# Performance work log

Hardware: AMD Instinct MI355X
Metric: run time of the kernel (lower is better)

Reference implementation:

```python
import jax, jax.numpy as jnp
import numpy as np
import math

B, T, D, H = 2, 2048, 2048, 16
HD = D // H  # head_dim = 128


def setup_inputs() -> dict:
    key = jax.random.key(0)
    ks = jax.random.split(key, 9)
    s = 1.0 / math.sqrt(D)
    return {
        "x": jax.random.normal(ks[0], (B, T, D), dtype=jnp.float32),
        "Wq": jax.random.normal(ks[1], (D, D), dtype=jnp.float32) * s,
        "bq": jax.random.normal(ks[2], (D,), dtype=jnp.float32) * 0.01,
        "Wk": jax.random.normal(ks[3], (D, D), dtype=jnp.float32) * s,
        "bk": jax.random.normal(ks[4], (D,), dtype=jnp.float32) * 0.01,
        "Wv": jax.random.normal(ks[5], (D, D), dtype=jnp.float32) * s,
        "bv": jax.random.normal(ks[6], (D,), dtype=jnp.float32) * 0.01,
        "Wo": jax.random.normal(ks[7], (D, D), dtype=jnp.float32) * s,
        "bo": jax.random.normal(ks[8], (D,), dtype=jnp.float32) * 0.01,
    }


def reference(x, Wq, bq, Wk, bk, Wv, bv, Wo, bo):
    b, t, c = x.shape
    # projections; split heads: (B,T,D) -> (B,H,T,HD)
    def split_heads(y):
        return y.reshape(b, t, H, HD).transpose(0, 2, 1, 3)

    q = split_heads(x @ Wq + bq)
    k = split_heads(x @ Wk + bk)
    v = split_heads(x @ Wv + bv)

    scale = 1.0 / math.sqrt(HD)
    attn = jnp.einsum('bhqd,bhkd->bhqk', q, k) * scale  # (B,H,T,T)
    # causal mask (prefill path: past_k is None)
    causal = jnp.tril(jnp.ones((t, t), dtype=bool))
    attn = jnp.where(causal, attn, -jnp.inf)
    attn = jax.nn.softmax(attn, axis=-1)
    out = jnp.einsum('bhqk,bhkd->bhqd', attn, v)  # (B,H,T,HD)
    out = out.transpose(0, 2, 1, 3).reshape(b, t, c)
    out = out @ Wo + bo
    return (out, k, v)
```

## Files before the change

kernel.cpp:

```cpp
#include <hip/hip_runtime.h>
#include <hip/hip_bf16.h>

#define B_ 2
#define T_ 2048
#define D_ 2048
#define H_ 16
#define HD_ 128
#define M_ 4096

typedef __attribute__((ext_vector_type(8))) short short8;
typedef __attribute__((ext_vector_type(8))) __bf16 bf16x8;
typedef __attribute__((ext_vector_type(4))) float f32x4;
typedef __attribute__((ext_vector_type(4))) unsigned uint32x4;

__device__ __forceinline__ short f2bf(float f) {
  unsigned u = __builtin_bit_cast(unsigned, f);
  u += 0x7fffu + ((u >> 16) & 1u);
  return (short)(u >> 16);
}

__device__ __forceinline__ unsigned cvtpk(float lo, float hi) {
  unsigned r;
  asm("v_cvt_pk_bf16_f32 %0, %1, %2" : "=v"(r) : "v"(lo), "v"(hi));
  return r;
}

__device__ __forceinline__ float ex2(float x) {
  float r;
  asm("v_exp_f32 %0, %1" : "=v"(r) : "v"(x));
  return r;
}

__device__ __forceinline__ void gl_lds16(const void* g, void* l) {
  __builtin_amdgcn_global_load_lds(
      (const __attribute__((address_space(1))) unsigned int*)g,
      (__attribute__((address_space(3))) unsigned int*)l, 16, 0, 0);
}

__device__ __forceinline__ f32x4 mfma_bf16(short8 a, short8 b, f32x4 c) {
  return __builtin_amdgcn_mfma_f32_16x16x32_bf16(
      __builtin_bit_cast(bf16x8, a), __builtin_bit_cast(bf16x8, b), c, 0, 0, 0);
}

__device__ __forceinline__ float2 sw16f(float x) {
  float a = x, bv;
  asm("v_mov_b32 %0, %1" : "=v"(bv) : "v"(x));
  asm("v_permlane16_swap_b32 %0, %1" : "+v"(a), "+v"(bv));
  return make_float2(a, bv);
}
__device__ __forceinline__ float2 sw32f(float x) {
  float a = x, bv;
  asm("v_mov_b32 %0, %1" : "=v"(bv) : "v"(x));
  asm("v_permlane32_swap_b32 %0, %1" : "+v"(a), "+v"(bv));
  return make_float2(a, bv);
}
__device__ __forceinline__ void sw16u(unsigned x, unsigned& e, unsigned& o) {
  unsigned a = x, bv;
  asm("v_mov_b32 %0, %1" : "=v"(bv) : "v"(x));
  asm("v_permlane16_swap_b32 %0, %1" : "+v"(a), "+v"(bv));
  e = a; o = bv;
}
__device__ __forceinline__ void pl32u(unsigned& a, unsigned& b) {
  asm("v_permlane32_swap_b32 %0, %1" : "+v"(a), "+v"(b));
}

__global__ void prep_fused(const float* __restrict__ Wq, const float* __restrict__ Wk,
                           const float* __restrict__ Wv, const float* __restrict__ Wo,
                           const float* __restrict__ x,
                           short* __restrict__ wqkv, short* __restrict__ wo,
                           short* __restrict__ xb) {
  int z = blockIdx.z;
  int tx = threadIdx.x, ty = threadIdx.y;
  if (z == 4) {
    int n4 = M_ * D_ / 4;
    int i = (blockIdx.y * 64 + blockIdx.x) * 256 + ty * 32 + tx;
    int stride = 64 * 64 * 256;
    for (; i < n4; i += stride) {
      float4 v = ((const float4*)x)[i];
      short4 s;
      s.x = f2bf(v.x); s.y = f2bf(v.y); s.z = f2bf(v.z); s.w = f2bf(v.w);
      ((short4*)xb)[i] = s;
    }
    return;
  }
  __shared__ float t[32][33];
  const float* W = z == 0 ? Wq : z == 1 ? Wk : z == 2 ? Wv : Wo;
  short* dst = z < 3 ? wqkv + (size_t)z * D_ * D_ : wo;
  int n0 = blockIdx.x * 32, k0 = blockIdx.y * 32;
#pragma unroll
  for (int j = 0; j < 4; ++j)
    t[ty + j * 8][tx] = W[(size_t)(k0 + ty + j * 8) * D_ + n0 + tx];
  __syncthreads();
#pragma unroll
  for (int j = 0; j < 4; ++j)
    dst[(size_t)(n0 + ty + j * 8) * D_ + k0 + tx] = f2bf(t[tx][ty + j * 8]);
}

__global__ __launch_bounds__(512, 2) void gemm_qkv(
    const short* __restrict__ A, const short* __restrict__ Bt,
    const float* __restrict__ b0, const float* __restrict__ b1,
    const float* __restrict__ b2,
    short* __restrict__ q_o, short* __restrict__ k_o,
    float* __restrict__ kf_o, float* __restrict__ vf_o,
    short* __restrict__ vt_o) {
  __shared__ __attribute__((aligned(16))) char lds[2][57344];
  const int K = D_, NT = K / 64;

  int d = blockIdx.x;
  int lg = (d & 7) * 64 + (d >> 3);
  int m0 = (lg & 15) * 256, n0 = (lg >> 4) * 192;

  int tid = threadIdx.x, lane = tid & 63, wid = tid >> 6;
  int wm = wid >> 2, wn = wid & 3;
  int lr = lane & 15, g = lane >> 4;

  int rowA = tid >> 2;
  int cA = ((((tid & 3) << 4) ^ (((rowA >> 1) & 3) << 4)) >> 1);
  const short* aS = A + (size_t)(m0 + rowA) * K + cA;
  int rowB = tid >> 3;
  int cB = ((((tid & 7) << 4) ^ ((rowB & 7) << 4)) >> 1);
  const short* bS = Bt + (size_t)(n0 + rowB) * K + cB;
  char* ldsb = (char*)lds;

  auto stageA = [&](int ts, int kh) {
    char* dst = ldsb + (ts & 1) * 57344 + kh * 16384 + tid * 16;
    const short* s = aS + ts * 64 + kh * 32;
    gl_lds16(s, dst);
    gl_lds16(s + (size_t)128 * K, dst + 8192);
  };
  auto stageB = [&](int ts) {
    char* dst = ldsb + (ts & 1) * 57344 + 32768 + tid * 16;
    const short* s = bS + ts * 64;
    gl_lds16(s, dst);
    gl_lds16(s + (size_t)64 * K, dst + 8192);
    gl_lds16(s + (size_t)128 * K, dst + 16384);
  };

  int swzA = (g * 16) ^ (((lr >> 1) & 3) << 4);
  int aoff = (wm * 128 + lr) * 64 + swzA;
  int boff0 = (wn * 48 + lr) * 128 + ((g * 16) ^ ((lr & 7) << 4));
  int boff1 = (wn * 48 + lr) * 128 + ((64 + g * 16) ^ ((lr & 7) << 4));

  f32x4 acc[8][3] = {};

  stageA(0, 0); stageB(0); stageA(0, 1); stageA(1, 0);
  asm volatile("s_waitcnt vmcnt(4)" ::: "memory");
  __builtin_amdgcn_s_barrier();
  __builtin_amdgcn_sched_barrier(0);

#pragma unroll 1
  for (int t = 0; t < NT; ++t) {
    const char* base = ldsb + (t & 1) * 57344;
    int t1 = (t + 1 < NT) ? t + 1 : NT - 1;
    int t2 = (t + 2 < NT) ? t + 2 : NT - 1;
    short8 afr[8], bfr[3];

#pragma unroll
    for (int mi = 0; mi < 8; ++mi) afr[mi] = *(const short8*)(base + aoff + mi * 1024);
#pragma unroll
    for (int ni = 0; ni < 3; ++ni) bfr[ni] = *(const short8*)(base + 32768 + boff0 + ni * 2048);
    stageA(t1, 1); stageB(t1);
    __builtin_amdgcn_s_setprio(1);
#pragma unroll
    for (int mi = 0; mi < 8; ++mi)
#pragma unroll
      for (int ni = 0; ni < 3; ++ni)
        acc[mi][ni] = mfma_bf16(afr[mi], bfr[ni], acc[mi][ni]);
    __builtin_amdgcn_s_setprio(0);
    asm volatile("s_waitcnt vmcnt(7)" ::: "memory");
    __builtin_amdgcn_s_barrier();
    __builtin_amdgcn_sched_barrier(0);

#pragma unroll
    for (int mi = 0; mi < 8; ++mi) afr[mi] = *(const short8*)(base + 16384 + aoff + mi * 1024);
#pragma unroll
    for (int ni = 0; ni < 3; ++ni) bfr[ni] = *(const short8*)(base + 32768 + boff1 + ni * 2048);
    stageA(t2, 0);
    __builtin_amdgcn_s_setprio(1);
#pragma unroll
    for (int mi = 0; mi < 8; ++mi)
#pragma unroll
      for (int ni = 0; ni < 3; ++ni)
        acc[mi][ni] = mfma_bf16(afr[mi], bfr[ni], acc[mi][ni]);
    __builtin_amdgcn_s_setprio(0);
    asm volatile("s_waitcnt vmcnt(2)" ::: "memory");
    __builtin_amdgcn_s_barrier();
    __builtin_amdgcn_sched_barrier(0);
  }

#pragma unroll
  for (int ni = 0; ni < 3; ++ni) {
    int gcb = n0 + wn * 48 + ni * 16;
    int region = gcb >> 11;
    int nc = (gcb & 2047) + lr;
    int hh = nc >> 7, hd = nc & 127;
    const float* bias = region == 0 ? b0 : region == 1 ? b1 : b2;
    float bv = bias[nc];
#pragma unroll
    for (int mi = 0; mi < 8; ++mi) {
      int gr0 = m0 + wm * 128 + mi * 16 + (g << 2);
      int bb = gr0 >> 11, tt0 = gr0 & 2047;
      size_t hbase = (size_t)(bb * H_ + hh);
      float v0 = acc[mi][ni][0] + bv;
      float v1 = acc[mi][ni][1] + bv;
      float v2 = acc[mi][ni][2] + bv;
      float v3 = acc[mi][ni][3] + bv;
      size_t ib = (hbase * T_ + tt0) * HD_ + hd;
      if (region == 0) {
        q_o[ib] = f2bf(v0); q_o[ib + HD_] = f2bf(v1);
        q_o[ib + 2 * HD_] = f2bf(v2); q_o[ib + 3 * HD_] = f2bf(v3);
      } else if (region == 1) {
        k_o[ib] = f2bf(v0); k_o[ib + HD_] = f2bf(v1);
        k_o[ib + 2 * HD_] = f2bf(v2); k_o[ib + 3 * HD_] = f2bf(v3);
        kf_o[ib] = v0; kf_o[ib + HD_] = v1;
        kf_o[ib + 2 * HD_] = v2; kf_o[ib + 3 * HD_] = v3;
      } else {
        vf_o[ib] = v0; vf_o[ib + HD_] = v1;
        vf_o[ib + 2 * HD_] = v2; vf_o[ib + 3 * HD_] = v3;
        short4 s4;
        s4.x = f2bf(v0); s4.y = f2bf(v1); s4.z = f2bf(v2); s4.w = f2bf(v3);
        *(short4*)&vt_o[(hbase * HD_ + hd) * T_ + tt0] = s4;
      }
    }
  }
}

__global__ __launch_bounds__(256, 2) void gemm_rb(
    const short* __restrict__ A, const short* __restrict__ Bt,
    const float* __restrict__ b0, float* __restrict__ f_o) {
  __shared__ __attribute__((aligned(16))) short lds[4][2][4096];
  const int K = D_, NT = K / 32;

  int nx = gridDim.x, nwg = nx * gridDim.y;
  int d = blockIdx.y * nx + blockIdx.x;
  int cpx = nwg >> 3;
  int lg = (d & 7) * cpx + (d >> 3);
  int m0 = (lg / nx) * 128, n0 = (lg % nx) * 128;

  int tid = threadIdx.x, lane = tid & 63, w = tid >> 6;
  int wm = w >> 1, wn = w & 1;
  int lr = lane & 15, g = lane >> 4;

  int o1 = tid * 16, o2 = 4096 + tid * 16;
  int row1 = tid >> 2, row2 = 64 + row1;
  int cb = (tid & 3) << 4;
  int c1 = (cb ^ (((row1 >> 1) & 3) << 4)) >> 1;
  int c2 = (cb ^ (((row2 >> 1) & 3) << 4)) >> 1;
  const short* aS1 = A + (size_t)(m0 + row1) * K + c1;
  const short* aS2 = A + (size_t)(m0 + row2) * K + c2;
  const short* bS1 = Bt + (size_t)(n0 + row1) * K + c1;
  const short* bS2 = Bt + (size_t)(n0 + row2) * K + c2;

  int aoff[4], boff[4];
#pragma unroll
  for (int i = 0; i < 4; ++i) {
    int ra = wm * 64 + i * 16 + lr;
    aoff[i] = ra * 64 + ((g * 16) ^ (((ra >> 1) & 3) << 4));
    int rb = wn * 64 + i * 16 + lr;
    boff[i] = rb * 64 + ((g * 16) ^ (((rb >> 1) & 3) << 4));
  }

  f32x4 acc[4][4] = {};

#pragma unroll
  for (int s = 0; s < 3; ++s) {
    char* la = (char*)&lds[s][0][0];
    char* lb = (char*)&lds[s][1][0];
    gl_lds16(aS1 + s * 32, la + o1);
    gl_lds16(aS2 + s * 32, la + o2);
    gl_lds16(bS1 + s * 32, lb + o1);
    gl_lds16(bS2 + s * 32, lb + o2);
  }
  asm volatile("s_waitcnt vmcnt(8)" ::: "memory");
  __builtin_amdgcn_s_barrier();
  __builtin_amdgcn_sched_barrier(0);

#pragma unroll 1
  for (int t4 = 0; t4 < NT; t4 += 4) {
#pragma unroll
    for (int p = 0; p < 4; ++p) {
      int t = t4 + p;
      {
        int ts = (t + 3 < NT) ? t + 3 : NT - 1;
        char* la = (char*)&lds[(p + 3) & 3][0][0];
        char* lb = (char*)&lds[(p + 3) & 3][1][0];
        gl_lds16(aS1 + ts * 32, la + o1);
        gl_lds16(aS2 + ts * 32, la + o2);
        gl_lds16(bS1 + ts * 32, lb + o1);
        gl_lds16(bS2 + ts * 32, lb + o2);
      }
      const char* la = (const char*)&lds[p][0][0];
      const char* lb = (const char*)&lds[p][1][0];
      short8 af[4], bfv[4];
#pragma unroll
      for (int i = 0; i < 4; ++i) {
        af[i] = *(const short8*)(la + aoff[i]);
        bfv[i] = *(const short8*)(lb + boff[i]);
      }
      __builtin_amdgcn_s_setprio(1);
#pragma unroll
      for (int mi = 0; mi < 4; ++mi)
#pragma unroll
        for (int ni = 0; ni < 4; ++ni)
          acc[mi][ni] = mfma_bf16(af[mi], bfv[ni], acc[mi][ni]);
      __builtin_amdgcn_s_setprio(0);
      asm volatile("s_waitcnt vmcnt(8)" ::: "memory");
      __builtin_amdgcn_s_barrier();
      __builtin_amdgcn_sched_barrier(0);
    }
  }

#pragma unroll
  for (int mi = 0; mi < 4; ++mi) {
#pragma unroll
    for (int ni = 0; ni < 4; ++ni) {
      int gr0 = m0 + wm * 64 + mi * 16 + (g << 2);
      int gc = n0 + wn * 64 + ni * 16 + lr;
      float bv = b0[gc];
#pragma unroll
      for (int r = 0; r < 4; ++r)
        f_o[(size_t)(gr0 + r) * D_ + gc] = acc[mi][ni][r] + bv;
    }
  }
}

__global__ __launch_bounds__(256, 2) void attn_fwd(
    const short* __restrict__ qb, const short* __restrict__ kb,
    const short* __restrict__ vtb, short* __restrict__ aob) {
  __shared__ __attribute__((aligned(16))) char kvlds[2][16384];

  int d = blockIdx.x;
  int bh = d & 31;
  int qt = 31 - (d >> 5);
  int tid = threadIdx.x, w = tid >> 6, lane = tid & 63;
  int lr = lane & 15, g = lane >> 4;
  const short* Q  = qb  + (size_t)bh * T_ * HD_;
  const short* Kp = kb  + (size_t)bh * T_ * HD_;
  const short* Vt = vtb + (size_t)bh * HD_ * T_;
  const float scale2 = 0.12751879202f;
  int b = bh >> 4, h = bh & 15;
  bool hi16 = (lane & 16) != 0;

  int oA = ((2 * w + 0) * 64 + lane) * 16;
  int oB = ((2 * w + 1) * 64 + lane) * 16;
  int rKA = oA >> 8, rKB = oB >> 8;
  size_t skA = (size_t)rKA * HD_ + (((oA & 255) ^ ((rKA & 7) << 4)) >> 1);
  size_t skB = (size_t)rKB * HD_ + (((oB & 255) ^ ((rKB & 7) << 4)) >> 1);
  int rVA = oA >> 6, rVB = oB >> 6;
  size_t svA = (size_t)rVA * T_ + (((oA & 63) ^ (((rVA >> 1) & 3) << 4)) >> 1);
  size_t svB = (size_t)rVB * T_ + (((oB & 63) ^ (((rVB >> 1) & 3) << 4)) >> 1);

  int q0 = qt * 64 + w * 16;
  int ntiles = 2 * qt + 2;

  {
    char* kd = &kvlds[0][0];
    char* vd = &kvlds[0][8192];
    gl_lds16(Kp + skA, kd + oA);
    gl_lds16(Kp + skB, kd + oB);
    gl_lds16(Vt + svA, vd + oA);
    gl_lds16(Vt + svB, vd + oB);
  }

  short8 qf[4];
#pragma unroll
  for (int kk = 0; kk < 4; ++kk)
    qf[kk] = *(const short8*)&Q[(size_t)(q0 + lr) * HD_ + kk * 32 + g * 8];

  f32x4 o[8] = {};
  float mrow = -1e30f, lrow = 0.f;
  __syncthreads();

#pragma unroll 1
  for (int t = 0; t < ntiles; ++t) {
    int kv0 = t * 32, buf = t & 1;
    if (t + 1 < ntiles) {
      char* kd = &kvlds[buf ^ 1][0];
      char* vd = &kvlds[buf ^ 1][8192];
      const short* Kn = Kp + (size_t)(kv0 + 32) * HD_;
      const short* Vn = Vt + (kv0 + 32);
      gl_lds16(Kn + skA, kd + oA);
      gl_lds16(Kn + skB, kd + oB);
      gl_lds16(Vn + svA, vd + oA);
      gl_lds16(Vn + svB, vd + oB);
    }
    if (kv0 < q0 + 16) {
      const char* kb_ = &kvlds[buf][0];
      const char* vb_ = &kvlds[buf][8192];
      short8 kf0[4], kf1[4], vf[8];
#pragma unroll
      for (int kk = 0; kk < 4; ++kk) {
        int cs = (kk * 64 + g * 16) ^ ((lr & 7) << 4);
        kf0[kk] = *(const short8*)(kb_ + (lr * 256 + cs));
        kf1[kk] = *(const short8*)(kb_ + ((16 + lr) * 256 + cs));
      }
#pragma unroll
      for (int f = 0; f < 8; ++f)
        vf[f] = *(const short8*)(vb_ + ((f * 16 + lr) * 64 +
                 ((g * 16) ^ (((lr >> 1) & 3) << 4))));

      f32x4 s0 = {}, s1 = {};
      __builtin_amdgcn_s_setprio(1);
#pragma unroll
      for (int kk = 0; kk < 4; ++kk) {
        s0 = mfma_bf16(kf0[kk], qf[kk], s0);
        s1 = mfma_bf16(kf1[kk], qf[kk], s1);
      }
      __builtin_amdgcn_s_setprio(0);

      float vv[8];
#pragma unroll
      for (int r = 0; r < 4; ++r) {
        vv[r] = s0[r] * scale2;
        vv[4 + r] = s1[r] * scale2;
      }
      if (kv0 + 31 > q0) {
        int qrow = q0 + lr;
#pragma unroll
        for (int r = 0; r < 4; ++r) {
          if (kv0 + 4 * g + r > qrow) vv[r] = -1e30f;
          if (kv0 + 16 + 4 * g + r > qrow) vv[4 + r] = -1e30f;
        }
      }

      float pm = vv[0];
#pragma unroll
      for (int i = 1; i < 8; ++i) pm = fmaxf(pm, vv[i]);
      { float2 tpm = sw32f(pm); pm = fmaxf(tpm.x, tpm.y); }
      { float2 tpm = sw16f(pm); pm = fmaxf(tpm.x, tpm.y); }

      bool rescale = !__all(pm - mrow <= 11.54f);
      float alpha = 1.0f;
      if (rescale) {
        float mnew = fmaxf(mrow, pm);
        alpha = ex2(mrow - mnew);
        mrow = mnew;
      }

      float p[8];
      float rs = 0.f;
#pragma unroll
      for (int i = 0; i < 8; ++i) { p[i] = ex2(vv[i] - mrow); rs += p[i]; }
      { float2 trs = sw32f(rs); rs = trs.x + trs.y; }
      { float2 trs = sw16f(rs); rs = trs.x + trs.y; }
      lrow = (rescale ? lrow * alpha : lrow) + rs;

      if (rescale) {
        float alr[4];
#pragma unroll
        for (int r = 0; r < 4; ++r) alr[r] = __shfl(alpha, 4 * g + r);
#pragma unroll
        for (int f = 0; f < 8; ++f)
#pragma unroll
          for (int r = 0; r < 4; ++r) o[f][r] *= alr[r];
      }

      unsigned w0 = cvtpk(p[0], p[1]), w1 = cvtpk(p[2], p[3]);
      unsigned w2 = cvtpk(p[4], p[5]), w3 = cvtpk(p[6], p[7]);
      unsigned e0, od0, e1, od1, e2, od2, e3, od3;
      sw16u(w0, e0, od0); sw16u(w1, e1, od1);
      sw16u(w2, e2, od2); sw16u(w3, e3, od3);
      unsigned F0 = e0,  S0 = e2;  pl32u(F0, S0);
      unsigned F1 = e1,  S1 = e3;  pl32u(F1, S1);
      unsigned F2 = od0, S2 = od2; pl32u(F2, S2);
      unsigned F3 = od1, S3 = od3; pl32u(F3, S3);
      uint32x4 paw = { hi16 ? S0 : F0, hi16 ? S1 : F1,
                       hi16 ? S2 : F2, hi16 ? S3 : F3 };
      short8 pa = __builtin_bit_cast(short8, paw);

      __builtin_amdgcn_s_setprio(1);
#pragma unroll
      for (int f = 0; f < 8; ++f) o[f] = mfma_bf16(pa, vf[f], o[f]);
      __builtin_amdgcn_s_setprio(0);
    }
    __syncthreads();
  }

  float inv = 1.0f / lrow;
  float invr[4];
#pragma unroll
  for (int r = 0; r < 4; ++r) invr[r] = __shfl(inv, 4 * g + r);
#pragma unroll
  for (int r = 0; r < 4; ++r) {
    int q = q0 + 4 * g + r;
    size_t rowoff = ((size_t)(b * T_ + q)) * D_ + h * HD_;
#pragma unroll
    for (int f = 0; f < 8; ++f)
      aob[rowoff + f * 16 + lr] = f2bf(o[f][r] * invr[r]);
  }
}

extern "C" void kernel_launch(void* const* d_in, const int* in_sizes, int n_in,
                              void* d_out, int out_size, void* d_ws, size_t ws_size,
                              hipStream_t stream) {
  const float* x  = (const float*)d_in[0];
  const float* Wq = (const float*)d_in[1];
  const float* bq = (const float*)d_in[2];
  const float* Wk = (const float*)d_in[3];
  const float* bk = (const float*)d_in[4];
  const float* Wv = (const float*)d_in[5];
  const float* bv = (const float*)d_in[6];
  const float* Wo = (const float*)d_in[7];
  const float* bo = (const float*)d_in[8];
  float* out  = (float*)d_out;
  float* kout = out + (size_t)M_ * D_;
  float* vout = kout + (size_t)M_ * D_;

  char* ws = (char*)d_ws;
  auto alloc = [&](size_t bytes) {
    char* p = ws;
    ws += (bytes + 255) & ~(size_t)255;
    return p;
  };
  short* xb    = (short*)alloc((size_t)M_ * D_ * 2);
  short* wqkvT = (short*)alloc((size_t)3 * D_ * D_ * 2);
  short* woT   = (short*)alloc((size_t)D_ * D_ * 2);
  short* qb    = (short*)alloc((size_t)M_ * D_ * 2);
  short* kb    = (short*)alloc((size_t)M_ * D_ * 2);
  short* vtb   = (short*)alloc((size_t)M_ * D_ * 2);
  short* aob = xb;

  dim3 tb(32, 8);
  prep_fused<<<dim3(64, 64, 5), tb, 0, stream>>>(Wq, Wk, Wv, Wo, x, wqkvT, woT, xb);

  gemm_qkv<<<512, 512, 0, stream>>>(xb, wqkvT, bq, bk, bv, qb, kb, kout, vout, vtb);
  attn_fwd<<<1024, 256, 0, stream>>>(qb, kb, vtb, aob);
  gemm_rb<<<dim3(16, 32), 256, 0, stream>>>(aob, woT, bo, out);
}
```

Before: 243.3 us.

## Rewrite output projection GEMM with 256x128 tiles, 8 waves, BK=64 double-buffering

Replaces the 128x128-tile, 4-wave output-projection GEMM with a 256x128-tile, 8-wave kernel that uses a K-step of 64 and a double-buffered LDS pipeline with split A-half staging. The grid drops from 512 to 256 workgroups, each doing more MFMA work per LDS load. The aim is better operand reuse and fewer barriers per K. The risk is fewer workgroups (256 for the GPU's CUs) and higher LDS use per block (96KB), which could limit occupancy or load balance.

Measured after the change: 240.8 us. About the same (-1.1%).

```diff
diff --git a/kernel.cpp b/kernel.cpp
--- a/kernel.cpp
+++ b/kernel.cpp
@@ -225,98 +225,100 @@
   }
 }
 
-__global__ __launch_bounds__(256, 2) void gemm_rb(
+__global__ __launch_bounds__(512, 2) void gemm_wo(
     const short* __restrict__ A, const short* __restrict__ Bt,
     const float* __restrict__ b0, float* __restrict__ f_o) {
-  __shared__ __attribute__((aligned(16))) short lds[4][2][4096];
-  const int K = D_, NT = K / 32;
-
-  int nx = gridDim.x, nwg = nx * gridDim.y;
-  int d = blockIdx.y * nx + blockIdx.x;
-  int cpx = nwg >> 3;
-  int lg = (d & 7) * cpx + (d >> 3);
-  int m0 = (lg / nx) * 128, n0 = (lg % nx) * 128;
-
-  int tid = threadIdx.x, lane = tid & 63, w = tid >> 6;
-  int wm = w >> 1, wn = w & 1;
+  __shared__ __attribute__((aligned(16))) char lds[2][49152];
+  const int K = D_, NT = K / 64;
+
+  int d = blockIdx.x;
+  int lg = (d & 7) * 32 + (d >> 3);
+  int m0 = (lg & 15) * 256, n0 = (lg >> 4) * 128;
+
+  int tid = threadIdx.x, lane = tid & 63, wid = tid >> 6;
+  int wm = wid >> 2, wn = wid & 3;
   int lr = lane & 15, g = lane >> 4;
 
-  int o1 = tid * 16, o2 = 4096 + tid * 16;
-  int row1 = tid >> 2, row2 = 64 + row1;
-  int cb = (tid & 3) << 4;
-  int c1 = (cb ^ (((row1 >> 1) & 3) << 4)) >> 1;
-  int c2 = (cb ^ (((row2 >> 1) & 3) << 4)) >> 1;
-  const short* aS1 = A + (size_t)(m0 + row1) * K + c1;
-  const short* aS2 = A + (size_t)(m0 + row2) * K + c2;
-  const short* bS1 = Bt + (size_t)(n0 + row1) * K + c1;
-  const short* bS2 = Bt + (size_t)(n0 + row2) * K + c2;
-
-  int aoff[4], boff[4];
-#pragma unroll
-  for (int i = 0; i < 4; ++i) {
-    int ra = wm * 64 + i * 16 + lr;
-    aoff[i] = ra * 64 + ((g * 16) ^ (((ra >> 1) & 3) << 4));
-    int rb = wn * 64 + i * 16 + lr;
-    boff[i] = rb * 64 + ((g * 16) ^ (((rb >> 1) & 3) << 4));
-  }
-
-  f32x4 acc[4][4] = {};
-
-#pragma unroll
-  for (int s = 0; s < 3; ++s) {
-    char* la = (char*)&lds[s][0][0];
-    char* lb = (char*)&lds[s][1][0];
-    gl_lds16(aS1 + s * 32, la + o1);
-    gl_lds16(aS2 + s * 32, la + o2);
-    gl_lds16(bS1 + s * 32, lb + o1);
-    gl_lds16(bS2 + s * 32, lb + o2);
-  }
-  asm volatile("s_waitcnt vmcnt(8)" ::: "memory");
+  int rowA = tid >> 2;
+  int cA = ((((tid & 3) << 4) ^ (((rowA >> 1) & 3) << 4)) >> 1);
+  const short* aS = A + (size_t)(m0 + rowA) * K + cA;
+  int rowB = tid >> 3;
+  int cB = ((((tid & 7) << 4) ^ ((rowB & 7) << 4)) >> 1);
+  const short* bS = Bt + (size_t)(n0 + rowB) * K + cB;
+  char* ldsb = (char*)lds;
+
+  auto stageA = [&](int ts, int kh) {
+    char* dst = ldsb + (ts & 1) * 49152 + kh * 16384 + tid * 16;
+    const short* s = aS + ts * 64 + kh * 32;
+    gl_lds16(s, dst);
+    gl_lds16(s + (size_t)128 * K, dst + 8192);
+  };
+  auto stageB = [&](int ts) {
+    char* dst = ldsb + (ts & 1) * 49152 + 32768 + tid * 16;
+    const short* s = bS + ts * 64;
+    gl_lds16(s, dst);
+    gl_lds16(s + (size_t)64 * K, dst + 8192);
+  };
+
+  int swzA = (g * 16) ^ (((lr >> 1) & 3) << 4);
+  int aoff = (wm * 128 + lr) * 64 + swzA;
+  int boff0 = (wn * 32 + lr) * 128 + ((g * 16) ^ ((lr & 7) << 4));
+  int boff1 = (wn * 32 + lr) * 128 + ((64 + g * 16) ^ ((lr & 7) << 4));
+
+  f32x4 acc[8][2] = {};
+
+  stageA(0, 0); stageB(0); stageA(0, 1); stageA(1, 0);
+  asm volatile("s_waitcnt vmcnt(2)" ::: "memory");
   __builtin_amdgcn_s_barrier();
   __builtin_amdgcn_sched_barrier(0);
 
 #pragma unroll 1
-  for (int t4 = 0; t4 < NT; t4 += 4) {
-#pragma unroll
-    for (int p = 0; p < 4; ++p) {
-      int t = t4 + p;
-      {
-        int ts = (t + 3 < NT) ? t + 3 : NT - 1;
-        char* la = (char*)&lds[(p + 3) & 3][0][0];
-        char* lb = (char*)&lds[(p + 3) & 3][1][0];
-        gl_lds16(aS1 + ts * 32, la + o1);
-        gl_lds16(aS2 + ts * 32, la + o2);
-        gl_lds16(bS1 + ts * 32, lb + o1);
-        gl_lds16(bS2 + ts * 32, lb + o2);
-      }
-      const char* la = (const char*)&lds[p][0][0];
-      const char* lb = (const char*)&lds[p][1][0];
-      short8 af[4], bfv[4];
-#pragma unroll
-      for (int i = 0; i < 4; ++i) {
-        af[i] = *(const short8*)(la + aoff[i]);
-        bfv[i] = *(const short8*)(lb + boff[i]);
-      }
-      __builtin_amdgcn_s_setprio(1);
-#pragma unroll
-      for (int mi = 0; mi < 4; ++mi)
-#pragma unroll
-        for (int ni = 0; ni < 4; ++ni)
-          acc[mi][ni] = mfma_bf16(af[mi], bfv[ni], acc[mi][ni]);
-      __builtin_amdgcn_s_setprio(0);
-      asm volatile("s_waitcnt vmcnt(8)" ::: "memory");
-      __builtin_amdgcn_s_barrier();
-      __builtin_amdgcn_sched_barrier(0);
-    }
-  }
-
-#pragma unroll
-  for (int mi = 0; mi < 4; ++mi) {
-#pragma unroll
-    for (int ni = 0; ni < 4; ++ni) {
-      int gr0 = m0 + wm * 64 + mi * 16 + (g << 2);
-      int gc = n0 + wn * 64 + ni * 16 + lr;
-      float bv = b0[gc];
+  for (int t = 0; t < NT; ++t) {
+    const char* base = ldsb + (t & 1) * 49152;
+    int t1 = (t + 1 < NT) ? t + 1 : NT - 1;
+    int t2 = (t + 2 < NT) ? t + 2 : NT - 1;
+    short8 afr[8], bfr[2];
+
+#pragma unroll
+    for (int mi = 0; mi < 8; ++mi) afr[mi] = *(const short8*)(base + aoff + mi * 1024);
+#pragma unroll
+    for (int ni = 0; ni < 2; ++ni) bfr[ni] = *(const short8*)(base + 32768 + boff0 + ni * 2048);
+    stageA(t1, 1); stageB(t1);
+    __builtin_amdgcn_s_setprio(1);
+#pragma unroll
+    for (int mi = 0; mi < 8; ++mi)
+#pragma unroll
+      for (int ni = 0; ni < 2; ++ni)
+        acc[mi][ni] = mfma_bf16(afr[mi], bfr[ni], acc[mi][ni]);
+    __builtin_amdgcn_s_setprio(0);
+    asm volatile("s_waitcnt vmcnt(6)" ::: "memory");
+    __builtin_amdgcn_s_barrier();
+    __builtin_amdgcn_sched_barrier(0);
+
+#pragma unroll
+    for (int mi = 0; mi < 8; ++mi) afr[mi] = *(const short8*)(base + 16384 + aoff + mi * 1024);
+#pragma unroll
+    for (int ni = 0; ni < 2; ++ni) bfr[ni] = *(const short8*)(base + 32768 + boff1 + ni * 2048);
+    stageA(t2, 0);
+    __builtin_amdgcn_s_setprio(1);
+#pragma unroll
+    for (int mi = 0; mi < 8; ++mi)
+#pragma unroll
+      for (int ni = 0; ni < 2; ++ni)
+        acc[mi][ni] = mfma_bf16(afr[mi], bfr[ni], acc[mi][ni]);
+    __builtin_amdgcn_s_setprio(0);
+    asm volatile("s_waitcnt vmcnt(2)" ::: "memory");
+    __builtin_amdgcn_s_barrier();
+    __builtin_amdgcn_sched_barrier(0);
+  }
+
+#pragma unroll
+  for (int ni = 0; ni < 2; ++ni) {
+    int gc = n0 + wn * 32 + ni * 16 + lr;
+    float bv = b0[gc];
+#pragma unroll
+    for (int mi = 0; mi < 8; ++mi) {
+      int gr0 = m0 + wm * 128 + mi * 16 + (g << 2);
 #pragma unroll
       for (int r = 0; r < 4; ++r)
         f_o[(size_t)(gr0 + r) * D_ + gc] = acc[mi][ni][r] + bv;
@@ -525,5 +527,5 @@
 
   gemm_qkv<<<512, 512, 0, stream>>>(xb, wqkvT, bq, bk, bv, qb, kb, kout, vout, vtb);
   attn_fwd<<<1024, 256, 0, stream>>>(qb, kb, vtb, aob);
-  gemm_rb<<<dim3(16, 32), 256, 0, stream>>>(aob, woT, bo, out);
-}
+  gemm_wo<<<256, 512, 0, stream>>>(aob, woT, bo, out);
+}
```
